# Kernel tuning notes

Measured on AMD Instinct MI355X. Metric: run time of the kernel, lower is better.

## Reference

```python
import jax, jax.numpy as jnp
import numpy as np

B = 256
N = 1024
K = 64
BASIS = 8
SINKHORN_ITERS = 1
TEMP = 0.2
EPS = 1e-5


def log_sinkhorn(log_alpha, n_iters=SINKHORN_ITERS, temperature=TEMP):
    la = log_alpha / temperature
    for _ in range(n_iters):
        la = la - jax.scipy.special.logsumexp(la, axis=-1, keepdims=True)
        la = la - jax.scipy.special.logsumexp(la, axis=-2, keepdims=True)
    return jnp.exp(la)


def setup_inputs() -> dict:
    key = jax.random.key(0)
    k1, k2, k3, k4 = jax.random.split(key, 4)
    x = jax.random.normal(k1, (B, N * K), dtype=jnp.float32)
    A_logits = 0.01 * jax.random.normal(k2, (N, N), dtype=jnp.float32)
    W_1 = 0.01 * jax.random.normal(k3, (N, BASIS), dtype=jnp.float32)
    W_V = 0.01 * jax.random.normal(k4, (BASIS, K, K), dtype=jnp.float32)
    gamma2 = jnp.ones((N,), dtype=jnp.float32)  # LayerNorm(N) weight
    beta2 = jnp.zeros((N,), dtype=jnp.float32)  # LayerNorm(N) bias
    return {"x": x, "A_logits": A_logits, "W_1": W_1, "W_V": W_V,
            "gamma2": gamma2, "beta2": beta2}


def layernorm(x, gamma, beta):
    mu = jnp.mean(x, axis=-1, keepdims=True)
    var = jnp.mean(jnp.square(x - mu), axis=-1, keepdims=True)
    return (x - mu) * jax.lax.rsqrt(var + EPS) * gamma + beta


def reference(x, A_logits, W_1, W_V, gamma2, beta2):
    x_reshaped = x.reshape(B, N, K)
    A = log_sinkhorn(A_logits)                       # [N, N] doubly-stochastic
    W_logits = jnp.einsum('tk,kde->tde', W_1, W_V)   # [N, K, K]
    W = log_sinkhorn(W_logits)                       # per-block doubly-stochastic
    x_local = jnp.einsum('bni,nio->bno', x_reshaped, W)  # N independent KxK GEMMs
    x_local = layernorm(jnp.transpose(x_local, (0, 2, 1)), gamma2, beta2)  # [B,K,N]
    x_global = x_local @ A                           # [B,K,N]
    x_global = jnp.transpose(x_global, (0, 2, 1))    # [B,N,K]
    return x_global.reshape(B, N * K)
```

## Files before the change

### kernel.cpp

```cpp
#include <hip/hip_runtime.h>
#include <hip/hip_fp16.h>
#include <math.h>

#define NDIM 1024
#define KDIM 64
#define BDIM 256
#define BKDIM 16384

typedef unsigned short u16;
typedef __attribute__((ext_vector_type(8))) short bf16x8;
typedef __attribute__((ext_vector_type(4))) short bf16x4;
typedef __attribute__((ext_vector_type(4))) float f32x4;

__device__ __forceinline__ float bf2f(u16 u) {
  union { unsigned u; float f; } x; x.u = ((unsigned)u) << 16; return x.f;
}
__device__ __forceinline__ u16 f2bf(float f) {
  union { float f; unsigned u; } x; x.f = f;
  unsigned u = x.u;
  u += 0x7fffu + ((u >> 16) & 1u);
  return (u16)(u >> 16);
}

__device__ __forceinline__ void async16(const u16* g, u16* s) {
  __builtin_amdgcn_global_load_lds(
      (const __attribute__((address_space(1))) unsigned int*)g,
      (__attribute__((address_space(3))) unsigned int*)s,
      16, 0, 0);
}

__global__ __launch_bounds__(256) void k_pre(const float* __restrict__ Alog,
                                             float* __restrict__ r,
                                             const float* __restrict__ W1,
                                             const float* __restrict__ WV,
                                             u16* __restrict__ Wt) {
  __shared__ float sred[256];
  __shared__ float sla[64 * 65];
  int t = threadIdx.x;
  if (blockIdx.x < 1024) {
    int m = blockIdx.x;
    float v[4], mx = -3.0e38f;
#pragma unroll
    for (int j = 0; j < 4; j++) {
      v[j] = Alog[m * NDIM + t + j * 256] * 5.0f;
      mx = fmaxf(mx, v[j]);
    }
    sred[t] = mx; __syncthreads();
    for (int s = 128; s > 0; s >>= 1) { if (t < s) sred[t] = fmaxf(sred[t], sred[t + s]); __syncthreads(); }
    float bm = sred[0]; __syncthreads();
    float sm = 0.f;
#pragma unroll
    for (int j = 0; j < 4; j++) sm += __expf(v[j] - bm);
    sred[t] = sm; __syncthreads();
    for (int s = 128; s > 0; s >>= 1) { if (t < s) sred[t] += sred[t + s]; __syncthreads(); }
    if (t == 0) r[m] = bm + __logf(sred[0]);
  } else {
    int tb = blockIdx.x - 1024;
    int d = t >> 2, q = t & 3;
    float w1[8];
#pragma unroll
    for (int k = 0; k < 8; k++) w1[k] = W1[tb * 8 + k];
    float la[16];
#pragma unroll
    for (int j = 0; j < 16; j++) la[j] = 0.f;
#pragma unroll
    for (int k = 0; k < 8; k++) {
      float wk = w1[k];
      const float4* base = (const float4*)&WV[k * 4096 + d * 64 + q * 16];
#pragma unroll
      for (int v = 0; v < 4; v++) {
        float4 f = base[v];
        la[v * 4 + 0] += wk * f.x; la[v * 4 + 1] += wk * f.y;
        la[v * 4 + 2] += wk * f.z; la[v * 4 + 3] += wk * f.w;
      }
    }
    float mx = -3.0e38f;
#pragma unroll
    for (int j = 0; j < 16; j++) { la[j] *= 5.0f; mx = fmaxf(mx, la[j]); }
    float sm = 0.f;
#pragma unroll
    for (int j = 0; j < 16; j++) sm += __expf(la[j] - mx);
    for (int off = 1; off < 4; off <<= 1) {
      float mo = __shfl_xor(mx, off), so = __shfl_xor(sm, off);
      float mn = fmaxf(mx, mo);
      sm = sm * __expf(mx - mn) + so * __expf(mo - mn);
      mx = mn;
    }
    float rl = mx + __logf(sm);
#pragma unroll
    for (int j = 0; j < 16; j++) sla[d * 65 + q * 16 + j] = la[j] - rl;
    __syncthreads();
    int e = t >> 2, jj = t & 3;
    float lb[16]; float m2 = -3.0e38f;
#pragma unroll
    for (int i = 0; i < 16; i++) { lb[i] = sla[(jj * 16 + i) * 65 + e]; m2 = fmaxf(m2, lb[i]); }
    float s2 = 0.f;
#pragma unroll
    for (int i = 0; i < 16; i++) s2 += __expf(lb[i] - m2);
    for (int off = 1; off < 4; off <<= 1) {
      float mo = __shfl_xor(m2, off), so = __shfl_xor(s2, off);
      float mn = fmaxf(m2, mo);
      s2 = s2 * __expf(m2 - mn) + so * __expf(mo - mn);
      m2 = mn;
    }
    float cl = m2 + __logf(s2);
#pragma unroll
    for (int i = 0; i < 16; i++)
      Wt[tb * 4096 + e * 64 + jj * 16 + i] = f2bf(__expf(lb[i] - cl));
  }
}

__global__ __launch_bounds__(512, 4) void k_gemm1d(const float* __restrict__ x,
                                                   const u16* __restrict__ Wt,
                                                   u16* __restrict__ xln) {
  int bx = blockIdx.x, bt = blockIdx.y, t = threadIdx.x;
  int n8 = (bx & 15) * 8 + (bx >> 4);
  int w = t >> 6, l = t & 63, q = l >> 4, lr = l & 15;
  int p = w & 3, h = w >> 2;
  int nb = n8 * 8 + h * 4;
  const float* xb = x + (size_t)(bt * 64 + p * 16 + lr) * 65536;
  f32x4 acc[4][4] = {};
#pragma unroll
  for (int np = 0; np < 4; np++) {
    int n = nb + np;
#pragma unroll
    for (int ks = 0; ks < 2; ks++) {
      const float* xr = xb + n * 64 + ks * 32 + q * 8;
      float4 v0 = *(const float4*)xr;
      float4 v1 = *(const float4*)(xr + 4);
      float vf[8] = {v0.x, v0.y, v0.z, v0.w, v1.x, v1.y, v1.z, v1.w};
      bf16x8 ah, al;
#pragma unroll
      for (int j = 0; j < 8; j++) {
        u16 hh = f2bf(vf[j]);
        ah[j] = (short)hh;
        al[j] = (short)f2bf(vf[j] - bf2f(hh));
      }
#pragma unroll
      for (int ni = 0; ni < 4; ni++) {
        bf16x8 bfr = *(const bf16x8*)&Wt[(size_t)n * 4096 + (ni * 16 + lr) * 64 + ks * 32 + q * 8];
        acc[np][ni] = __builtin_amdgcn_mfma_f32_16x16x32_bf16(ah, bfr, acc[np][ni], 0, 0, 0);
        acc[np][ni] = __builtin_amdgcn_mfma_f32_16x16x32_bf16(al, bfr, acc[np][ni], 0, 0, 0);
      }
    }
  }
#pragma unroll
  for (int ni = 0; ni < 4; ni++) {
#pragma unroll
    for (int reg = 0; reg < 4; reg++) {
      int bk = (bt * 64 + p * 16 + q * 4 + reg) * 64 + ni * 16 + lr;
      bf16x4 o;
#pragma unroll
      for (int np = 0; np < 4; np++) o[np] = (short)f2bf(acc[np][ni][reg]);
      *(bf16x4*)&xln[(size_t)bk * 1024 + nb] = o;
    }
  }
}

__global__ __launch_bounds__(256) void k_post(const float* __restrict__ Alog,
                                              const float* __restrict__ r,
                                              const float* __restrict__ g2,
                                              const float* __restrict__ b2,
                                              u16* __restrict__ Dt,
                                              float* __restrict__ gAc,
                                              float* __restrict__ bAc,
                                              const u16* __restrict__ xln,
                                              float* __restrict__ e1,
                                              float* __restrict__ e2,
                                              float* __restrict__ e3) {
  __shared__ float sred[256];
  int t = threadIdx.x;
  if (blockIdx.x < 1024) {
    int n = blockIdx.x;
    float v[4], mx = -3.0e38f;
#pragma unroll
    for (int j = 0; j < 4; j++) {
      int m = t + j * 256;
      v[j] = Alog[m * NDIM + n] * 5.0f - r[m];
      mx = fmaxf(mx, v[j]);
    }
    sred[t] = mx; __syncthreads();
    for (int s = 128; s > 0; s >>= 1) { if (t < s) sred[t] = fmaxf(sred[t], sred[t + s]); __syncthreads(); }
    float bm = sred[0]; __syncthreads();
    float sm = 0.f;
#pragma unroll
    for (int j = 0; j < 4; j++) sm += __expf(v[j] - bm);
    sred[t] = sm; __syncthreads();
    for (int s = 128; s > 0; s >>= 1) { if (t < s) sred[t] += sred[t + s]; __syncthreads(); }
    float cn = bm + __logf(sred[0]);
    float ga = 0.f, ba = 0.f;
#pragma unroll
    for (int j = 0; j < 4; j++) {
      int m = t + j * 256;
      float e = __expf(v[j] - cn);
      float gm = g2[m];
      Dt[n * NDIM + m] = f2bf(gm * (e - 0.0009765625f));
      ga += gm * e; ba += b2[m] * e;
    }
    __syncthreads();
    sred[t] = ga; __syncthreads();
    for (int s = 128; s > 0; s >>= 1) { if (t < s) sred[t] += sred[t + s]; __syncthreads(); }
    if (t == 0) gAc[n] = sred[0];
    __syncthreads();
    sred[t] = ba; __syncthreads();
    for (int s = 128; s > 0; s >>= 1) { if (t < s) sred[t] += sred[t + s]; __syncthreads(); }
    if (t == 0) bAc[n] = sred[0];
  } else {
    int row = (blockIdx.x - 1024) * 16 + (t >> 4);
    int c = t & 15;
    const u16* xr = xln + (size_t)row * 1024 + c * 8;
    float S = 0.f, Q = 0.f, W = 0.f;
#pragma unroll
    for (int j = 0; j < 8; j++) {
      bf16x8 v = *(const bf16x8*)&xr[j * 128];
      const float* gp = g2 + j * 128 + c * 8;
      float4 g0 = *(const float4*)gp;
      float4 g1 = *(const float4*)(gp + 4);
      float gg[8] = {g0.x, g0.y, g0.z, g0.w, g1.x, g1.y, g1.z, g1.w};
#pragma unroll
      for (int k = 0; k < 8; k++) {
        float f = bf2f((u16)v[k]);
        S += f; Q += f * f; W += f * gg[k];
      }
    }
#pragma unroll
    for (int off = 1; off < 16; off <<= 1) {
      S += __shfl_xor(S, off);
      Q += __shfl_xor(Q, off);
      W += __shfl_xor(W, off);
    }
    if (c == 0) {
      float m_ = S * (1.0f / 1024.0f);
      float var = Q * (1.0f / 1024.0f) - m_ * m_;
      float a = rsqrtf(var + 1e-5f);
      e1[row] = a;
      e2[row] = a * W * (1.0f / 1024.0f);
      e3[row] = -a * m_;
    }
  }
}

__global__ __launch_bounds__(256) void k_gemm2g(const u16* __restrict__ Dt,
                                                const u16* __restrict__ xln,
                                                const float* __restrict__ e1,
                                                const float* __restrict__ e2,
                                                const float* __restrict__ e3,
                                                const float* __restrict__ gAc,
                                                const float* __restrict__ bAc,
                                                float* __restrict__ out) {
  __shared__ __align__(16) u16 lA[128 * 64];
  __shared__ __align__(16) u16 lB[128 * 64];
  int bkt = blockIdx.x, n2t = blockIdx.y;
  int t = threadIdx.x, w = t >> 6, l = t & 63;
  int q = l >> 4, lr = l & 15;
  int rr = l >> 3;
  int cc = (l & 7) ^ rr;
  const u16* gAp = Dt  + (size_t)(n2t * 128) * NDIM + cc * 8;
  const u16* gBp = xln + (size_t)(bkt * 128) * NDIM + cc * 8;
  f32x4 acc[4][4] = {};
  for (int kt = 0; kt < 16; kt++) {
#pragma unroll
    for (int j = 0; j < 4; j++) {
      int ci = j * 4 + w;
      int row = ci * 8 + rr;
      async16(gAp + (size_t)row * NDIM + kt * 64, &lA[ci * 512 + l * 8]);
      async16(gBp + (size_t)row * NDIM + kt * 64, &lB[ci * 512 + l * 8]);
    }
    __syncthreads();
#pragma unroll
    for (int ks = 0; ks < 2; ks++) {
      int pc = ((ks * 4 + q) ^ (lr & 7)) * 8;
      bf16x8 af[4], bfr[4];
#pragma unroll
      for (int mi = 0; mi < 4; mi++)
        af[mi] = *(const bf16x8*)&lA[((w >> 1) * 64 + mi * 16 + lr) * 64 + pc];
#pragma unroll
      for (int ni = 0; ni < 4; ni++)
        bfr[ni] = *(const bf16x8*)&lB[((w & 1) * 64 + ni * 16 + lr) * 64 + pc];
#pragma unroll
      for (int mi = 0; mi < 4; mi++)
#pragma unroll
        for (int ni = 0; ni < 4; ni++)
          acc[mi][ni] = __builtin_amdgcn_mfma_f32_16x16x32_bf16(af[mi], bfr[ni], acc[mi][ni], 0, 0, 0);
    }
    __syncthreads();
  }
  float* sE = (float*)lA;
  if (t < 128) {
    sE[t]       = e1[bkt * 128 + t];
    sE[128 + t] = e2[bkt * 128 + t];
    sE[256 + t] = e3[bkt * 128 + t];
    sE[384 + t] = gAc[n2t * 128 + t];
    sE[512 + t] = bAc[n2t * 128 + t];
  }
  __syncthreads();
  float a1v[4], a2v[4], a3v[4];
#pragma unroll
  for (int ni = 0; ni < 4; ni++) {
    int bkl = (w & 1) * 64 + ni * 16 + lr;
    a1v[ni] = sE[bkl]; a2v[ni] = sE[128 + bkl]; a3v[ni] = sE[256 + bkl];
  }
  int bkb = bkt * 128 + (w & 1) * 64 + lr;
#pragma unroll
  for (int mi = 0; mi < 4; mi++) {
    __builtin_amdgcn_sched_barrier(0);
#pragma unroll
    for (int reg = 0; reg < 4; reg++) {
      int n2l = (w >> 1) * 64 + mi * 16 + q * 4 + reg;
      float gg = sE[384 + n2l], bb = sE[512 + n2l];
      int n2 = n2t * 128 + n2l;
#pragma unroll
      for (int ni = 0; ni < 4; ni++) {
        int bk = bkb + ni * 16;
        int b = bk >> 6, o = bk & 63;
        out[(size_t)b * 65536 + n2 * 64 + o] =
            a1v[ni] * acc[mi][ni][reg] + a2v[ni] + a3v[ni] * gg + bb;
      }
    }
  }
}

extern "C" void kernel_launch(void* const* d_in, const int* in_sizes, int n_in,
                              void* d_out, int out_size, void* d_ws, size_t ws_size,
                              hipStream_t stream) {
  const float* x    = (const float*)d_in[0];
  const float* Alog = (const float*)d_in[1];
  const float* W1   = (const float*)d_in[2];
  const float* WV   = (const float*)d_in[3];
  const float* g2   = (const float*)d_in[4];
  const float* b2   = (const float*)d_in[5];
  float* out = (float*)d_out;
  char* ws = (char*)d_ws;

  u16*   xln = (u16*)(ws);
  u16*   Wt  = (u16*)(ws + 33554432ull);
  float* e1  = (float*)(ws + 33554432ull);
  float* e2  = (float*)(ws + 33619968ull);
  float* e3  = (float*)(ws + 33685504ull);
  u16*   Dt  = (u16*)(ws + 41943040ull);
  float* r   = (float*)(ws + 44040192ull);
  float* gAc = (float*)(ws + 44044288ull);
  float* bAc = (float*)(ws + 44048384ull);

  k_pre<<<dim3(2048), dim3(256), 0, stream>>>(Alog, r, W1, WV, Wt);
  k_gemm1d<<<dim3(128, 4), dim3(512), 0, stream>>>(x, Wt, xln);
  k_post<<<dim3(2048), dim3(256), 0, stream>>>(Alog, r, g2, b2, Dt, gAc, bAc, xln, e1, e2, e3);
  k_gemm2g<<<dim3(128, 8), dim3(256), 0, stream>>>(Dt, xln, e1, e2, e3, gAc, bAc, out);
}
```

Measured before the change: 224.2 us.

## Double-buffer LDS tiles in the second GEMM with a K-step of 32

Restructures the A·x GEMM main loop from single-buffered 64-wide K tiles to double-buffered 32-wide K tiles. The loads for the next tile are issued before the MFMAs on the current tile, so global-to-LDS traffic can overlap compute. This also drops from two barriers per 64-wide K step to one barrier per 32-wide step. Total LDS use stays the same, but there are twice as many iterations with less MFMA work between barriers, and the XOR swizzle changes from 8-way to 4-way.

After: 232.3 us. +3.6%, slower.

```diff
diff --git a/kernel.cpp b/kernel.cpp
--- a/kernel.cpp
+++ b/kernel.cpp
@@ -240,7 +240,7 @@
   }
 }
 
-__global__ __launch_bounds__(256) void k_gemm2g(const u16* __restrict__ Dt,
+__global__ __launch_bounds__(256) void k_gemm2h(const u16* __restrict__ Dt,
                                                 const u16* __restrict__ xln,
                                                 const float* __restrict__ e1,
                                                 const float* __restrict__ e2,
@@ -248,44 +248,54 @@
                                                 const float* __restrict__ gAc,
                                                 const float* __restrict__ bAc,
                                                 float* __restrict__ out) {
-  __shared__ __align__(16) u16 lA[128 * 64];
-  __shared__ __align__(16) u16 lB[128 * 64];
+  __shared__ __align__(16) u16 lA[2][128 * 32];
+  __shared__ __align__(16) u16 lB[2][128 * 32];
   int bkt = blockIdx.x, n2t = blockIdx.y;
   int t = threadIdx.x, w = t >> 6, l = t & 63;
   int q = l >> 4, lr = l & 15;
-  int rr = l >> 3;
-  int cc = (l & 7) ^ rr;
-  const u16* gAp = Dt  + (size_t)(n2t * 128) * NDIM + cc * 8;
-  const u16* gBp = xln + (size_t)(bkt * 128) * NDIM + cc * 8;
+  const u16* gA0 = Dt  + (size_t)(n2t * 128) * NDIM;
+  const u16* gB0 = xln + (size_t)(bkt * 128) * NDIM;
+  int srow = w * 16 + (l >> 2);
+  int scol = (((l & 3) ^ ((l >> 2) & 3))) * 8;
+  int sdst = (w * 16) * 32 + l * 8;
+  int pc = (q ^ (lr & 3)) * 8;
+
   f32x4 acc[4][4] = {};
-  for (int kt = 0; kt < 16; kt++) {
-#pragma unroll
-    for (int j = 0; j < 4; j++) {
-      int ci = j * 4 + w;
-      int row = ci * 8 + rr;
-      async16(gAp + (size_t)row * NDIM + kt * 64, &lA[ci * 512 + l * 8]);
-      async16(gBp + (size_t)row * NDIM + kt * 64, &lB[ci * 512 + l * 8]);
-    }
+#pragma unroll
+  for (int j = 0; j < 2; j++) {
+    async16(gA0 + (size_t)(j * 64 + srow) * NDIM + scol, &lA[0][j * 2048 + sdst]);
+    async16(gB0 + (size_t)(j * 64 + srow) * NDIM + scol, &lB[0][j * 2048 + sdst]);
+  }
+  __syncthreads();
+
+#pragma unroll 2
+  for (int kt = 0; kt < 32; kt++) {
+    int cur = kt & 1;
+    if (kt < 31) {
+      int nxt = cur ^ 1;
+      int mo = (kt + 1) * 32 + scol;
+#pragma unroll
+      for (int j = 0; j < 2; j++) {
+        async16(gA0 + (size_t)(j * 64 + srow) * NDIM + mo, &lA[nxt][j * 2048 + sdst]);
+        async16(gB0 + (size_t)(j * 64 + srow) * NDIM + mo, &lB[nxt][j * 2048 + sdst]);
+      }
+    }
+    bf16x8 af[4], bfr[4];
+#pragma unroll
+    for (int mi = 0; mi < 4; mi++)
+      af[mi] = *(const bf16x8*)&lA[cur][((w >> 1) * 64 + mi * 16 + lr) * 32 + pc];
+#pragma unroll
+    for (int ni = 0; ni < 4; ni++)
+      bfr[ni] = *(const bf16x8*)&lB[cur][((w & 1) * 64 + ni * 16 + lr) * 32 + pc];
+#pragma unroll
+    for (int mi = 0; mi < 4; mi++)
+#pragma unroll
+      for (int ni = 0; ni < 4; ni++)
+        acc[mi][ni] = __builtin_amdgcn_mfma_f32_16x16x32_bf16(af[mi], bfr[ni], acc[mi][ni], 0, 0, 0);
     __syncthreads();
-#pragma unroll
-    for (int ks = 0; ks < 2; ks++) {
-      int pc = ((ks * 4 + q) ^ (lr & 7)) * 8;
-      bf16x8 af[4], bfr[4];
-#pragma unroll
-      for (int mi = 0; mi < 4; mi++)
-        af[mi] = *(const bf16x8*)&lA[((w >> 1) * 64 + mi * 16 + lr) * 64 + pc];
-#pragma unroll
-      for (int ni = 0; ni < 4; ni++)
-        bfr[ni] = *(const bf16x8*)&lB[((w & 1) * 64 + ni * 16 + lr) * 64 + pc];
-#pragma unroll
-      for (int mi = 0; mi < 4; mi++)
-#pragma unroll
-        for (int ni = 0; ni < 4; ni++)
-          acc[mi][ni] = __builtin_amdgcn_mfma_f32_16x16x32_bf16(af[mi], bfr[ni], acc[mi][ni], 0, 0, 0);
-    }
-    __syncthreads();
-  }
-  float* sE = (float*)lA;
+  }
+
+  float* sE = (float*)&lA[0][0];
   if (t < 128) {
     sE[t]       = e1[bkt * 128 + t];
     sE[128 + t] = e2[bkt * 128 + t];
@@ -345,5 +355,5 @@
   k_pre<<<dim3(2048), dim3(256), 0, stream>>>(Alog, r, W1, WV, Wt);
   k_gemm1d<<<dim3(128, 4), dim3(512), 0, stream>>>(x, Wt, xln);
   k_post<<<dim3(2048), dim3(256), 0, stream>>>(Alog, r, g2, b2, Dt, gAc, bAc, xln, e1, e2, e3);
-  k_gemm2g<<<dim3(128, 8), dim3(256), 0, stream>>>(Dt, xln, e1, e2, e3, gAc, bAc, out);
-}
+  k_gemm2h<<<dim3(128, 8), dim3(256), 0, stream>>>(Dt, xln, e1, e2, e3, gAc, bAc, out);
+}
```
